# Kernel tuning notes

Measured on AMD Instinct MI355X. Metric: run time of the kernel, lower is better.

Reference implementation:

```python
import jax, jax.numpy as jnp
import numpy as np

VEC = 512
HEADS = 8
HEAD = VEC // HEADS  # 64
B, L = 4, 2048
EPS = 1e-3  # keras LayerNormalization default epsilon


def setup_inputs() -> dict:
    key = jax.random.key(0)
    ks = jax.random.split(key, 9)
    return {
        "query": jax.random.normal(ks[0], (B, L, VEC), dtype=jnp.float32),
        "key": jax.random.normal(ks[1], (B, L, VEC), dtype=jnp.float32),
        "value": jax.random.normal(ks[2], (B, L, VEC), dtype=jnp.float32),
        "query_mask": jnp.ones((B, L), dtype=jnp.float32),
        "value_mask": jnp.ones((B, L), dtype=jnp.float32),
        "Wq": jax.random.normal(ks[3], (HEADS, VEC, HEAD), dtype=jnp.float32) * 0.02,
        "Wk": jax.random.normal(ks[4], (HEADS, VEC, HEAD), dtype=jnp.float32) * 0.02,
        "Wv": jax.random.normal(ks[5], (HEADS, VEC, HEAD), dtype=jnp.float32) * 0.02,
        "gamma": jnp.ones((VEC,), dtype=jnp.float32),
        "beta": jnp.zeros((VEC,), dtype=jnp.float32),
    }


def reference(query, key, value, query_mask, value_mask, Wq, Wk, Wv, gamma, beta):
    b, l, v = query.shape
    h, _, d = Wq.shape
    # batched per-head projections (equivalent to the per-head Dense loop)
    Q = jnp.einsum("blv,hvd->bhld", query, Wq)
    K = jnp.einsum("blv,hvd->bhld", key, Wk)
    V = jnp.einsum("blv,hvd->bhld", value, Wv)
    scores = jnp.einsum("bhld,bhmd->bhlm", Q, K) / jnp.sqrt(jnp.float32(d))
    att = jax.nn.softmax(scores, axis=-1)
    # post-softmax multiplicative masks (faithful to the original)
    tri = jnp.tril(jnp.ones((l, l), dtype=att.dtype))  # causal triangle mask
    att = att * tri
    att = att * (query_mask[:, None, :, None] * value_mask[:, None, None, :])
    head = jnp.einsum("bhlm,bhmd->bhld", att, V)
    # concat heads along feature dim: (B,L,H*D)
    x = jnp.transpose(head, (0, 2, 1, 3)).reshape(b, l, h * d)
    # dropout inactive at inference; residual + LayerNorm (eps=1e-3)
    y = x + query
    mean = jnp.mean(y, axis=-1, keepdims=True)
    var = jnp.mean(jnp.square(y - mean), axis=-1, keepdims=True)
    return (y - mean) / jnp.sqrt(var + EPS) * gamma + beta
```

## Files before the change

### kernel.cpp

```cpp
#include <hip/hip_runtime.h>
#include <hip/hip_bf16.h>

#define BSZ 4
#define LSEQ 2048
#define VECD 512
#define NH 8
#define HD 64

typedef __attribute__((ext_vector_type(8))) short bf16x8;
typedef __attribute__((ext_vector_type(4))) short short4v;
typedef __attribute__((ext_vector_type(8))) short short8v;
typedef __attribute__((ext_vector_type(4))) float f32x4;
typedef __attribute__((ext_vector_type(16))) float f32x16;

__device__ inline short f2bf(float f) {
    union { float f; unsigned u; } v; v.f = f;
    unsigned u = v.u;
    u += 0x7fffu + ((u >> 16) & 1u);
    return (short)(u >> 16);
}

__device__ inline unsigned cvtpk_bf16(float lo, float hi) {
    unsigned r;
    asm volatile("v_cvt_pk_bf16_f32 %0, %1, %2" : "=v"(r) : "v"(lo), "v"(hi));
    return r;
}

__device__ inline float exp2a(float v) {
    float r;
    asm("v_exp_f32 %0, %1" : "=v"(r) : "v"(v));
    return r;
}

__device__ inline void plswap(unsigned &a, unsigned &b) {
    asm volatile("v_permlane32_swap_b32 %0, %1" : "+v"(a), "+v"(b));
}

__device__ inline void gll16(const void* g, void* l) {
    __builtin_amdgcn_global_load_lds(
        (const __attribute__((address_space(1))) unsigned int*)g,
        (__attribute__((address_space(3))) unsigned int*)l, 16, 0, 0);
}

__launch_bounds__(256)
__global__ void w_kernel(const float* __restrict__ Wq, const float* __restrict__ Wk,
                         const float* __restrict__ Wv, short* __restrict__ WT) {
    __shared__ short T[64][72];
    const int bi = blockIdx.x;
    const int z = bi >> 3, h = bi & 7;
    const float* W = ((z == 0) ? Wq : (z == 1) ? Wk : Wv) + (size_t)h * VECD * HD;
    short* out = WT + (size_t)z * 512 * 512 + (size_t)h * 64 * 512;

    const int tid = threadIdx.x;
    for (int kt = 0; kt < 8; kt++) {
        int k0 = kt * 64;
        int r = tid >> 2, seg = tid & 3;
        for (int j = 0; j < 4; j++) {
            float4 v = *(const float4*)(W + (size_t)(k0 + r) * HD + seg * 16 + j * 4);
            T[seg * 16 + j * 4 + 0][r] = f2bf(v.x);
            T[seg * 16 + j * 4 + 1][r] = f2bf(v.y);
            T[seg * 16 + j * 4 + 2][r] = f2bf(v.z);
            T[seg * 16 + j * 4 + 3][r] = f2bf(v.w);
        }
        __syncthreads();
        int d = tid >> 2, ks = tid & 3;
        *(short8v*)(out + (size_t)d * 512 + k0 + ks * 16) = *(const short8v*)&T[d][ks * 16];
        *(short8v*)(out + (size_t)d * 512 + k0 + ks * 16 + 8) = *(const short8v*)&T[d][ks * 16 + 8];
        __syncthreads();
    }
}

__launch_bounds__(256, 3)
__global__ void proj_kernel(const float* __restrict__ q_in, const float* __restrict__ k_in,
                            const float* __restrict__ v_in, const short* __restrict__ WT,
                            short* __restrict__ Qp, short* __restrict__ Kp,
                            short* __restrict__ Vp) {
    __shared__ short As[128 * 64];
    __shared__ short Bs[128 * 64];

    const int z = blockIdx.z;
    const float* in = (z == 0) ? q_in : (z == 1) ? k_in : v_in;
    short* out      = (z == 0) ? Qp   : (z == 1) ? Kp   : Vp;
    const float sc  = (z == 0) ? 0.18033688011112042f : 1.0f;
    const short* wt = WT + (size_t)z * 512 * 512;

    const int tid  = threadIdx.x;
    const int lane = tid & 63;
    const int w    = tid >> 6;
    const int r0   = blockIdx.x * 128;
    const int n0   = blockIdx.y * 128;

    const int row16 = lane & 15;
    const int grp   = lane >> 4;
    const int wm    = (w >> 1) * 64;
    const int wn    = (w & 1) * 64;

    f32x4 acc[4][4];
    for (int i = 0; i < 4; i++)
        for (int j = 0; j < 4; j++) acc[i][j] = (f32x4)0.f;

    for (int k0 = 0; k0 < VECD; k0 += 64) {
        for (int i = 0; i < 8; i++) {
            int id = tid + 256 * i;
            int m = id >> 4, kc4 = id & 15;
            float4 v = *(const float4*)(in + (size_t)(r0 + m) * VECD + k0 + kc4 * 4);
            int c = kc4 >> 1, half = kc4 & 1;
            uint2 p;
            p.x = cvtpk_bf16(v.x, v.y);
            p.y = cvtpk_bf16(v.z, v.w);
            *(uint2*)&As[m * 64 + (c ^ (m & 7)) * 8 + half * 4] = p;
        }
        for (int i = 0; i < 4; i++) {
            int id = tid + 256 * i;
            int n = id >> 3, c = id & 7;
            gll16(wt + (size_t)(n0 + n) * 512 + k0 + ((c ^ (n & 7)) * 8),
                  (void*)(Bs + (w * 64 + 256 * i) * 8));
        }
        __syncthreads();

        for (int kc = 0; kc < 2; kc++) {
            bf16x8 a[4], b[4];
            for (int mt = 0; mt < 4; mt++) {
                int row = wm + mt * 16 + row16;
                int cg = kc * 4 + grp;
                a[mt] = *(const bf16x8*)&As[row * 64 + (cg ^ (row & 7)) * 8];
            }
            for (int nt = 0; nt < 4; nt++) {
                int row = wn + nt * 16 + row16;
                int cg = kc * 4 + grp;
                b[nt] = *(const bf16x8*)&Bs[row * 64 + (cg ^ (row & 7)) * 8];
            }
            for (int mt = 0; mt < 4; mt++)
                for (int nt = 0; nt < 4; nt++)
                    acc[mt][nt] = __builtin_amdgcn_mfma_f32_16x16x32_bf16(a[mt], b[nt], acc[mt][nt], 0, 0, 0);
        }
        __syncthreads();
    }

    for (int mt = 0; mt < 4; mt++)
        for (int r = 0; r < 4; r++) {
            int m = r0 + wm + mt * 16 + grp * 4 + r;
            int b = m >> 11, l = m & (LSEQ - 1);
            for (int nt = 0; nt < 4; nt++) {
                int n = n0 + wn + nt * 16 + row16;
                int h = n >> 6, d = n & 63;
                out[(((size_t)b * NH + h) * LSEQ + l) * HD + d] = f2bf(acc[mt][nt][r] * sc);
            }
        }
}

__launch_bounds__(256)
__global__ void vt_kernel(const short* __restrict__ Vp, short* __restrict__ VpT) {
    __shared__ short T[64][72];
    const int bh = blockIdx.y;
    const int l0 = blockIdx.x * 64;
    const short* src = Vp + (size_t)bh * LSEQ * HD + (size_t)l0 * HD;
    short* dst = VpT + (size_t)bh * HD * LSEQ;

    const int tid = threadIdx.x;
    const int row = tid >> 2, c16 = tid & 3;
    *(bf16x8*)&T[row][c16 * 16]     = *(const bf16x8*)(src + row * HD + c16 * 16);
    *(bf16x8*)&T[row][c16 * 16 + 8] = *(const bf16x8*)(src + row * HD + c16 * 16 + 8);
    __syncthreads();

    const int d = tid >> 2, seg = tid & 3;
    short8v o0, o1;
    for (int j = 0; j < 8; j++) o0[j] = T[seg * 16 + j][d];
    for (int j = 0; j < 8; j++) o1[j] = T[seg * 16 + 8 + j][d];
    *(short8v*)(dst + (size_t)d * LSEQ + l0 + seg * 16)     = o0;
    *(short8v*)(dst + (size_t)d * LSEQ + l0 + seg * 16 + 8) = o1;
}

__launch_bounds__(256, 4)
__global__ void attn_kernel(const short* __restrict__ Qp, const short* __restrict__ Kp,
                            const short* __restrict__ VpT,
                            const float* __restrict__ qmask, const float* __restrict__ vmask,
                            float* __restrict__ x) {
    __shared__ char smem[16384 + 2 * 2 * 32 * 4];
    short* Ks  = (short*)smem;
    short* VTs = (short*)(smem + 8192);
    float* Dd  = (float*)(smem + 16384);
    float* Ex  = (float*)smem;

    const int tid  = threadIdx.x;
    const int lane = tid & 63;
    const int w    = tid >> 6;
    const int pair = w >> 1;
    const int mh   = w & 1;

    const int ii  = blockIdx.x + 32 * blockIdx.y;
    const int swz = (ii & 7) * 128 + (ii >> 3);
    const int x31 = swz & 31;
    const int bh  = swz >> 5;
    const int b   = bh >> 3;
    const int h   = bh & 7;

    const int t  = (pair == 0) ? x31 : (63 - x31);
    const int kd = t >> 1;
    const int kv = (63 - x31) >> 1;
    const int qbase = t * 32;

    const size_t base   = (size_t)bh * LSEQ * HD;
    const size_t vtbase = (size_t)bh * HD * LSEQ;

    const int l31  = lane & 31;
    const int hsel = lane >> 5;
    const int lq   = qbase + l31;

    bf16x8 q[4];
    #pragma unroll
    for (int ks = 0; ks < 4; ks++)
        q[ks] = *(const bf16x8*)(Qp + base + (size_t)lq * HD + ks * 16 + hsel * 8);

    f32x16 o0 = (f32x16)0.f, o1 = (f32x16)0.f;
    float dsum = 0.f;

    bf16x8 kr[2], vr[2];
    auto loadTile = [&](int k) {
        const short* ksrc = Kp + base + (size_t)(k * 64) * HD;
        #pragma unroll
        for (int i = 0; i < 2; i++) {
            int id = tid + 256 * i;
            int row = id >> 3, c = id & 7;
            int cs = c ^ (row & 7) ^ ((row >> 3) & 7);
            kr[i] = *(const bf16x8*)(ksrc + row * HD + cs * 8);
            if (k <= kv)
                vr[i] = *(const bf16x8*)(VpT + vtbase + (size_t)row * LSEQ + k * 64 + cs * 8);
        }
    };
    auto writeTile = [&](int k) {
        #pragma unroll
        for (int i = 0; i < 2; i++) {
            int id = tid + 256 * i;
            *(bf16x8*)&Ks[id * 8] = kr[i];
            if (k <= kv) *(bf16x8*)&VTs[id * 8] = vr[i];
        }
    };

    loadTile(0);
    writeTile(0);

    const int mrow = mh * 32 + l31;
    const int msw  = (mrow & 7) ^ ((mrow >> 3) & 7);

    for (int k = 0; k < 32; ++k) {
        __syncthreads();
        if (k < 31) loadTile(k + 1);

        f32x16 s = (f32x16)0.f;
        bf16x8 kf[4];
        #pragma unroll
        for (int ks = 0; ks < 4; ks++)
            kf[ks] = *(const bf16x8*)&Ks[mrow * 64 + ((ks * 2 + hsel) ^ msw) * 8];
        #pragma unroll
        for (int ks = 0; ks < 4; ks++)
            s = __builtin_amdgcn_mfma_f32_32x32x16_bf16(kf[ks], q[ks], s, 0, 0, 0);

        float e[16];
        #pragma unroll
        for (int r = 0; r < 16; r++) {
            e[r] = exp2a(s[r]);
            dsum += e[r];
        }

        if (k <= kd) {
            #pragma unroll
            for (int g = 0; g < 4; g++) {
                int mb = k * 64 + mh * 32 + 8 * g + 4 * hsel;
                float4 vm = *(const float4*)(vmask + b * LSEQ + mb);
                float m0v = vm.x, m1v = vm.y, m2v = vm.z, m3v = vm.w;
                if (k == kd) {
                    m0v = (mb + 0 <= lq) ? m0v : 0.f;
                    m1v = (mb + 1 <= lq) ? m1v : 0.f;
                    m2v = (mb + 2 <= lq) ? m2v : 0.f;
                    m3v = (mb + 3 <= lq) ? m3v : 0.f;
                }
                e[4 * g + 0] *= m0v; e[4 * g + 1] *= m1v;
                e[4 * g + 2] *= m2v; e[4 * g + 3] *= m3v;
            }

            #pragma unroll
            for (int ks2 = 0; ks2 < 2; ks2++) {
                int b0 = 8 * ks2;
                unsigned pk0 = cvtpk_bf16(e[b0 + 0], e[b0 + 1]);
                unsigned pk1 = cvtpk_bf16(e[b0 + 2], e[b0 + 3]);
                unsigned pk2 = cvtpk_bf16(e[b0 + 4], e[b0 + 5]);
                unsigned pk3 = cvtpk_bf16(e[b0 + 6], e[b0 + 7]);
                plswap(pk2, pk0);
                plswap(pk3, pk1);
                union { unsigned u[4]; bf16x8 v; } pu;
                pu.u[0] = pk0; pu.u[1] = pk1; pu.u[2] = pk2; pu.u[3] = pk3;

                int chunk = mh * 4 + ks2 * 2 + hsel;
                {
                    int drow = l31;
                    bf16x8 vb = *(const bf16x8*)&VTs[drow * 64 +
                        ((chunk ^ (drow & 7) ^ ((drow >> 3) & 7))) * 8];
                    o0 = __builtin_amdgcn_mfma_f32_32x32x16_bf16(pu.v, vb, o0, 0, 0, 0);
                }
                {
                    int drow = 32 + l31;
                    bf16x8 vb = *(const bf16x8*)&VTs[drow * 64 +
                        ((chunk ^ (drow & 7) ^ ((drow >> 3) & 7))) * 8];
                    o1 = __builtin_amdgcn_mfma_f32_32x32x16_bf16(pu.v, vb, o1, 0, 0, 0);
                }
            }
        }

        __syncthreads();
        if (k < 31) writeTile(k + 1);
    }

    dsum += __shfl_xor(dsum, 32, 64);
    if (lane < 32) Dd[pair * 64 + mh * 32 + l31] = dsum;
    __syncthreads();

    {
        const int wbuf = (pair * 2 + (1 - mh)) * 1024;
        #pragma unroll
        for (int r = 0; r < 16; r++) {
            int ql = (r & 3) + 8 * (r >> 2) + 4 * hsel;
            Ex[wbuf + ql * 32 + l31] = (mh == 0) ? o1[r] : o0[r];
        }
    }
    __syncthreads();

    {
        const int rbuf = (pair * 2 + mh) * 1024;
        #pragma unroll
        for (int r = 0; r < 16; r++) {
            int ql = (r & 3) + 8 * (r >> 2) + 4 * hsel;
            float own = (mh == 0) ? o0[r] : o1[r];
            float val = own + Ex[rbuf + ql * 32 + l31];
            float den = Dd[pair * 64 + ql] + Dd[pair * 64 + 32 + ql];
            int lqr = qbase + ql;
            float inv = qmask[b * LSEQ + lqr] / den;
            x[((size_t)b * LSEQ + lqr) * VECD + h * HD + mh * 32 + l31] = val * inv;
        }
    }
}

__launch_bounds__(256)
__global__ void ln_kernel(const float* __restrict__ x, const float* __restrict__ q,
                          const float* __restrict__ gamma, const float* __restrict__ beta,
                          float* __restrict__ out) {
    const int tid  = threadIdx.x;
    const int lane = tid & 63;
    const int w    = tid >> 6;
    const size_t row = (size_t)blockIdx.x * 4 + w;

    const float* xr = x + row * VECD + lane * 8;
    const float* qr = q + row * VECD + lane * 8;
    float4 a0 = *(const float4*)xr;
    float4 a1 = *(const float4*)(xr + 4);
    float4 b0 = *(const float4*)qr;
    float4 b1 = *(const float4*)(qr + 4);
    float y[8] = { a0.x + b0.x, a0.y + b0.y, a0.z + b0.z, a0.w + b0.w,
                   a1.x + b1.x, a1.y + b1.y, a1.z + b1.z, a1.w + b1.w };

    float s = 0.f;
    for (int j = 0; j < 8; j++) s += y[j];
    for (int off = 1; off < 64; off <<= 1) s += __shfl_xor(s, off, 64);
    float mean = s * (1.f / 512.f);

    float v = 0.f;
    for (int j = 0; j < 8; j++) { float d = y[j] - mean; v += d * d; }
    for (int off = 1; off < 64; off <<= 1) v += __shfl_xor(v, off, 64);
    float inv = rsqrtf(v * (1.f / 512.f) + 1e-3f);

    float4 g0 = *(const float4*)(gamma + lane * 8);
    float4 g1 = *(const float4*)(gamma + lane * 8 + 4);
    float4 e0 = *(const float4*)(beta + lane * 8);
    float4 e1 = *(const float4*)(beta + lane * 8 + 4);

    float4 o0, o1;
    o0.x = (y[0] - mean) * inv * g0.x + e0.x;
    o0.y = (y[1] - mean) * inv * g0.y + e0.y;
    o0.z = (y[2] - mean) * inv * g0.z + e0.z;
    o0.w = (y[3] - mean) * inv * g0.w + e0.w;
    o1.x = (y[4] - mean) * inv * g1.x + e1.x;
    o1.y = (y[5] - mean) * inv * g1.y + e1.y;
    o1.z = (y[6] - mean) * inv * g1.z + e1.z;
    o1.w = (y[7] - mean) * inv * g1.w + e1.w;
    *(float4*)(out + row * VECD + lane * 8) = o0;
    *(float4*)(out + row * VECD + lane * 8 + 4) = o1;
}

extern "C" void kernel_launch(void* const* d_in, const int* in_sizes, int n_in,
                              void* d_out, int out_size, void* d_ws, size_t ws_size,
                              hipStream_t stream) {
    const float* query = (const float*)d_in[0];
    const float* key   = (const float*)d_in[1];
    const float* value = (const float*)d_in[2];
    const float* qmask = (const float*)d_in[3];
    const float* vmask = (const float*)d_in[4];
    const float* Wq    = (const float*)d_in[5];
    const float* Wk    = (const float*)d_in[6];
    const float* Wv    = (const float*)d_in[7];
    const float* gamma = (const float*)d_in[8];
    const float* beta  = (const float*)d_in[9];

    const size_t QKV_ELTS = (size_t)BSZ * NH * LSEQ * HD;
    short* Qp = (short*)d_ws;
    short* Kp = Qp + QKV_ELTS;
    short* Vp = Kp + QKV_ELTS;
    float* x  = (float*)(Vp + QKV_ELTS);
    short* WT = (short*)(x + (size_t)BSZ * LSEQ * VECD);
    short* VpT = WT + (size_t)3 * 512 * 512;

    w_kernel<<<24, 256, 0, stream>>>(Wq, Wk, Wv, WT);
    proj_kernel<<<dim3(64, 4, 3), 256, 0, stream>>>(query, key, value, WT, Qp, Kp, Vp);
    vt_kernel<<<dim3(32, 32), 256, 0, stream>>>(Vp, VpT);
    attn_kernel<<<dim3(32, 32), 256, 0, stream>>>(Qp, Kp, VpT, qmask, vmask, x);
    ln_kernel<<<2048, 256, 0, stream>>>(x, query, gamma, beta, (float*)d_out);
}
```

Before: 107.3 us.

## Double attention K/V tile to 128 keys and store intermediate output as bf16

The attention kernel now stages 128-key K and V^T tiles per iteration in twice the shared memory, running two 64-key sub-steps per barrier pair. This halves the number of __syncthreads and tile-load phases. The attention output x is also written as bf16 instead of fp32, which halves its write and its read by the LayerNorm kernel. In exchange, the larger LDS footprint may reduce occupancy, and the bf16 intermediate adds rounding before the residual add.

New measurement: 274.1 us. 2.55x slower.

```diff
diff --git a/kernel.cpp b/kernel.cpp
--- a/kernel.cpp
+++ b/kernel.cpp
@@ -175,11 +175,11 @@
 __global__ void attn_kernel(const short* __restrict__ Qp, const short* __restrict__ Kp,
                             const short* __restrict__ VpT,
                             const float* __restrict__ qmask, const float* __restrict__ vmask,
-                            float* __restrict__ x) {
-    __shared__ char smem[16384 + 2 * 2 * 32 * 4];
+                            short* __restrict__ x) {
+    __shared__ char smem[32768 + 2 * 2 * 32 * 4];
     short* Ks  = (short*)smem;
-    short* VTs = (short*)(smem + 8192);
-    float* Dd  = (float*)(smem + 16384);
+    short* VTs = (short*)(smem + 16384);
+    float* Dd  = (float*)(smem + 32768);
     float* Ex  = (float*)smem;
 
     const int tid  = threadIdx.x;
@@ -215,100 +215,109 @@
     f32x16 o0 = (f32x16)0.f, o1 = (f32x16)0.f;
     float dsum = 0.f;
 
-    bf16x8 kr[2], vr[2];
-    auto loadTile = [&](int k) {
-        const short* ksrc = Kp + base + (size_t)(k * 64) * HD;
+    bf16x8 kr[4], vr[4];
+    auto loadTile = [&](int kt) {
+        const short* ksrc = Kp + base + (size_t)(kt * 128) * HD;
+        const bool needV = (2 * kt <= kv);
         #pragma unroll
-        for (int i = 0; i < 2; i++) {
+        for (int i = 0; i < 4; i++) {
             int id = tid + 256 * i;
             int row = id >> 3, c = id & 7;
             int cs = c ^ (row & 7) ^ ((row >> 3) & 7);
             kr[i] = *(const bf16x8*)(ksrc + row * HD + cs * 8);
-            if (k <= kv)
-                vr[i] = *(const bf16x8*)(VpT + vtbase + (size_t)row * LSEQ + k * 64 + cs * 8);
+            if (needV) {
+                int d = id >> 4, ch = id & 15;
+                int cv = ch ^ (d & 7) ^ ((d >> 3) & 7);
+                vr[i] = *(const bf16x8*)(VpT + vtbase + (size_t)d * LSEQ + kt * 128 + cv * 8);
+            }
         }
     };
-    auto writeTile = [&](int k) {
+    auto writeTile = [&](int kt) {
+        const bool needV = (2 * kt <= kv);
         #pragma unroll
-        for (int i = 0; i < 2; i++) {
+        for (int i = 0; i < 4; i++) {
             int id = tid + 256 * i;
             *(bf16x8*)&Ks[id * 8] = kr[i];
-            if (k <= kv) *(bf16x8*)&VTs[id * 8] = vr[i];
+            if (needV) *(bf16x8*)&VTs[id * 8] = vr[i];
         }
     };
 
     loadTile(0);
     writeTile(0);
 
-    const int mrow = mh * 32 + l31;
-    const int msw  = (mrow & 7) ^ ((mrow >> 3) & 7);
-
-    for (int k = 0; k < 32; ++k) {
-        __syncthreads();
-        if (k < 31) loadTile(k + 1);
-
-        f32x16 s = (f32x16)0.f;
-        bf16x8 kf[4];
+    for (int kt = 0; kt < 16; ++kt) {
+        __syncthreads();
+        if (kt < 15) loadTile(kt + 1);
+
         #pragma unroll
-        for (int ks = 0; ks < 4; ks++)
-            kf[ks] = *(const bf16x8*)&Ks[mrow * 64 + ((ks * 2 + hsel) ^ msw) * 8];
-        #pragma unroll
-        for (int ks = 0; ks < 4; ks++)
-            s = __builtin_amdgcn_mfma_f32_32x32x16_bf16(kf[ks], q[ks], s, 0, 0, 0);
-
-        float e[16];
-        #pragma unroll
-        for (int r = 0; r < 16; r++) {
-            e[r] = exp2a(s[r]);
-            dsum += e[r];
-        }
-
-        if (k <= kd) {
+        for (int st2 = 0; st2 < 2; ++st2) {
+            const int kk = 2 * kt + st2;
+            const int mrow = st2 * 64 + mh * 32 + l31;
+            const int msw  = (mrow & 7) ^ ((mrow >> 3) & 7);
+
+            f32x16 s = (f32x16)0.f;
+            bf16x8 kf[4];
             #pragma unroll
-            for (int g = 0; g < 4; g++) {
-                int mb = k * 64 + mh * 32 + 8 * g + 4 * hsel;
-                float4 vm = *(const float4*)(vmask + b * LSEQ + mb);
-                float m0v = vm.x, m1v = vm.y, m2v = vm.z, m3v = vm.w;
-                if (k == kd) {
-                    m0v = (mb + 0 <= lq) ? m0v : 0.f;
-                    m1v = (mb + 1 <= lq) ? m1v : 0.f;
-                    m2v = (mb + 2 <= lq) ? m2v : 0.f;
-                    m3v = (mb + 3 <= lq) ? m3v : 0.f;
+            for (int ks = 0; ks < 4; ks++)
+                kf[ks] = *(const bf16x8*)&Ks[mrow * 64 + ((ks * 2 + hsel) ^ msw) * 8];
+            #pragma unroll
+            for (int ks = 0; ks < 4; ks++)
+                s = __builtin_amdgcn_mfma_f32_32x32x16_bf16(kf[ks], q[ks], s, 0, 0, 0);
+
+            float e[16];
+            #pragma unroll
+            for (int r = 0; r < 16; r++) {
+                e[r] = exp2a(s[r]);
+                dsum += e[r];
+            }
+
+            if (kk <= kd) {
+                #pragma unroll
+                for (int g = 0; g < 4; g++) {
+                    int mb = kk * 64 + mh * 32 + 8 * g + 4 * hsel;
+                    float4 vm = *(const float4*)(vmask + b * LSEQ + mb);
+                    float m0v = vm.x, m1v = vm.y, m2v = vm.z, m3v = vm.w;
+                    if (kk == kd) {
+                        m0v = (mb + 0 <= lq) ? m0v : 0.f;
+                        m1v = (mb + 1 <= lq) ? m1v : 0.f;
+                        m2v = (mb + 2 <= lq) ? m2v : 0.f;
+                        m3v = (mb + 3 <= lq) ? m3v : 0.f;
+                    }
+                    e[4 * g + 0] *= m0v; e[4 * g + 1] *= m1v;
+                    e[4 * g + 2] *= m2v; e[4 * g + 3] *= m3v;
                 }
-                e[4 * g + 0] *= m0v; e[4 * g + 1] *= m1v;
-                e[4 * g + 2] *= m2v; e[4 * g + 3] *= m3v;
-            }
-
-            #pragma unroll
-            for (int ks2 = 0; ks2 < 2; ks2++) {
-                int b0 = 8 * ks2;
-                unsigned pk0 = cvtpk_bf16(e[b0 + 0], e[b0 + 1]);
-                unsigned pk1 = cvtpk_bf16(e[b0 + 2], e[b0 + 3]);
-                unsigned pk2 = cvtpk_bf16(e[b0 + 4], e[b0 + 5]);
-                unsigned pk3 = cvtpk_bf16(e[b0 + 6], e[b0 + 7]);
-                plswap(pk2, pk0);
-                plswap(pk3, pk1);
-                union { unsigned u[4]; bf16x8 v; } pu;
-                pu.u[0] = pk0; pu.u[1] = pk1; pu.u[2] = pk2; pu.u[3] = pk3;
-
-                int chunk = mh * 4 + ks2 * 2 + hsel;
-                {
-                    int drow = l31;
-                    bf16x8 vb = *(const bf16x8*)&VTs[drow * 64 +
-                        ((chunk ^ (drow & 7) ^ ((drow >> 3) & 7))) * 8];
-                    o0 = __builtin_amdgcn_mfma_f32_32x32x16_bf16(pu.v, vb, o0, 0, 0, 0);
+
+                #pragma unroll
+                for (int ks2 = 0; ks2 < 2; ks2++) {
+                    int b0 = 8 * ks2;
+                    unsigned pk0 = cvtpk_bf16(e[b0 + 0], e[b0 + 1]);
+                    unsigned pk1 = cvtpk_bf16(e[b0 + 2], e[b0 + 3]);
+                    unsigned pk2 = cvtpk_bf16(e[b0 + 4], e[b0 + 5]);
+                    unsigned pk3 = cvtpk_bf16(e[b0 + 6], e[b0 + 7]);
+                    plswap(pk2, pk0);
+                    plswap(pk3, pk1);
+                    union { unsigned u[4]; bf16x8 v; } pu;
+                    pu.u[0] = pk0; pu.u[1] = pk1; pu.u[2] = pk2; pu.u[3] = pk3;
+
+                    int chunk = st2 * 8 + mh * 4 + ks2 * 2 + hsel;
+                    {
+                        int drow = l31;
+                        int cv = chunk ^ (drow & 7) ^ ((drow >> 3) & 7);
+                        bf16x8 vb = *(const bf16x8*)&VTs[drow * 128 + cv * 8];
+                        o0 = __builtin_amdgcn_mfma_f32_32x32x16_bf16(pu.v, vb, o0, 0, 0, 0);
+                    }
+                    {
+                        int drow = 32 + l31;
+                        int cv = chunk ^ (drow & 7) ^ ((drow >> 3) & 7);
+                        bf16x8 vb = *(const bf16x8*)&VTs[drow * 128 + cv * 8];
+                        o1 = __builtin_amdgcn_mfma_f32_32x32x16_bf16(pu.v, vb, o1, 0, 0, 0);
+                    }
                 }
-                {
-                    int drow = 32 + l31;
-                    bf16x8 vb = *(const bf16x8*)&VTs[drow * 64 +
-                        ((chunk ^ (drow & 7) ^ ((drow >> 3) & 7))) * 8];
-                    o1 = __builtin_amdgcn_mfma_f32_32x32x16_bf16(pu.v, vb, o1, 0, 0, 0);
-                }
-            }
-        }
-
-        __syncthreads();
-        if (k < 31) writeTile(k + 1);
+            }
+        }
+
+        __syncthreads();
+        if (kt < 15) writeTile(kt + 1);
     }
 
     dsum += __shfl_xor(dsum, 32, 64);
@@ -335,13 +344,13 @@
             float den = Dd[pair * 64 + ql] + Dd[pair * 64 + 32 + ql];
             int lqr = qbase + ql;
             float inv = qmask[b * LSEQ + lqr] / den;
-            x[((size_t)b * LSEQ + lqr) * VECD + h * HD + mh * 32 + l31] = val * inv;
+            x[((size_t)b * LSEQ + lqr) * VECD + h * HD + mh * 32 + l31] = f2bf(val * inv);
         }
     }
 }
 
 __launch_bounds__(256)
-__global__ void ln_kernel(const float* __restrict__ x, const float* __restrict__ q,
+__global__ void ln_kernel(const short* __restrict__ x, const float* __restrict__ q,
                           const float* __restrict__ gamma, const float* __restrict__ beta,
                           float* __restrict__ out) {
     const int tid  = threadIdx.x;
@@ -349,14 +358,18 @@
     const int w    = tid >> 6;
     const size_t row = (size_t)blockIdx.x * 4 + w;
 
-    const float* xr = x + row * VECD + lane * 8;
+    short8v xs = *(const short8v*)(x + row * VECD + lane * 8);
     const float* qr = q + row * VECD + lane * 8;
-    float4 a0 = *(const float4*)xr;
-    float4 a1 = *(const float4*)(xr + 4);
     float4 b0 = *(const float4*)qr;
     float4 b1 = *(const float4*)(qr + 4);
-    float y[8] = { a0.x + b0.x, a0.y + b0.y, a0.z + b0.z, a0.w + b0.w,
-                   a1.x + b1.x, a1.y + b1.y, a1.z + b1.z, a1.w + b1.w };
+    float xb[8];
+    #pragma unroll
+    for (int j = 0; j < 8; j++) {
+        union { unsigned u; float f; } c; c.u = ((unsigned)(unsigned short)xs[j]) << 16;
+        xb[j] = c.f;
+    }
+    float y[8] = { xb[0] + b0.x, xb[1] + b0.y, xb[2] + b0.z, xb[3] + b0.w,
+                   xb[4] + b1.x, xb[5] + b1.y, xb[6] + b1.z, xb[7] + b1.w };
 
     float s = 0.f;
     for (int j = 0; j < 8; j++) s += y[j];
@@ -404,8 +417,8 @@
     short* Qp = (short*)d_ws;
     short* Kp = Qp + QKV_ELTS;
     short* Vp = Kp + QKV_ELTS;
-    float* x  = (float*)(Vp + QKV_ELTS);
-    short* WT = (short*)(x + (size_t)BSZ * LSEQ * VECD);
+    short* x  = Vp + QKV_ELTS;
+    short* WT = x + QKV_ELTS;
     short* VpT = WT + (size_t)3 * 512 * 512;
 
     w_kernel<<<24, 256, 0, stream>>>(Wq, Wk, Wv, WT);
```
